# Kernel optimization log

Measured on AMD Instinct MI355X. Metric: run time of the kernel, lower is better.

The kernel has to match this reference:

```python
import jax, jax.numpy as jnp
import numpy as np

HIDDEN = 3072
HEADS = 24
HEAD_DIM = HIDDEN // HEADS  # 128
MLP_HIDDEN = 4 * HIDDEN     # 12288
IMG_LEN = 1024
TXT_LEN = 256
L = IMG_LEN + TXT_LEN
B = 1
EPS = 1e-6


def setup_inputs() -> dict:
    key = jax.random.key(0)
    ks = jax.random.split(key, 12)
    x = jax.random.normal(ks[0], (B, L, HIDDEN), jnp.float32)
    vec = jax.random.normal(ks[1], (B, HIDDEN), jnp.float32)
    # RoPE tables: real cos/sin of position * inv_freq, repeated over pairs (full head_dim)
    inv_freq = 1.0 / (10000.0 ** (np.arange(0, HEAD_DIM, 2, dtype=np.float32) / HEAD_DIM))
    theta = np.arange(IMG_LEN, dtype=np.float32)[:, None] * inv_freq[None, :]  # [img_len, D/2]
    theta = np.repeat(theta, 2, axis=-1)  # [img_len, D]
    freqs_cos = jnp.asarray(np.cos(theta))[None, :, None, :]  # [1, img_len, 1, D]
    freqs_sin = jnp.asarray(np.sin(theta))[None, :, None, :]
    s = 0.02
    mod_w = jax.random.normal(ks[2], (HIDDEN, 3 * HIDDEN), jnp.float32) * s
    mod_b = jnp.zeros((3 * HIDDEN,), jnp.float32)
    w1 = jax.random.normal(ks[3], (HIDDEN, 3 * HIDDEN + MLP_HIDDEN), jnp.float32) * s
    b1 = jnp.zeros((3 * HIDDEN + MLP_HIDDEN,), jnp.float32)
    w2 = jax.random.normal(ks[4], (HIDDEN + MLP_HIDDEN, HIDDEN), jnp.float32) * s
    b2 = jnp.zeros((HIDDEN,), jnp.float32)
    qn_w = jnp.ones((HEAD_DIM,), jnp.float32)
    kn_w = jnp.ones((HEAD_DIM,), jnp.float32)
    cu_seqlens_q = jnp.array([0, IMG_LEN, L], jnp.int32)
    cu_seqlens_kv = jnp.array([0, IMG_LEN, L], jnp.int32)
    return {"x": x, "vec": vec, "freqs_cos": freqs_cos, "freqs_sin": freqs_sin,
            "mod_w": mod_w, "mod_b": mod_b, "w1": w1, "b1": b1, "w2": w2, "b2": b2,
            "qn_w": qn_w, "kn_w": kn_w, "img_len": IMG_LEN,
            "cu_seqlens_q": cu_seqlens_q, "cu_seqlens_kv": cu_seqlens_kv}


def _layernorm(x):  # elementwise_affine=False
    mu = jnp.mean(x, axis=-1, keepdims=True)
    var = jnp.mean(jnp.square(x - mu), axis=-1, keepdims=True)
    return (x - mu) * jax.lax.rsqrt(var + EPS)


def _rmsnorm(x, w):
    ms = jnp.mean(jnp.square(x), axis=-1, keepdims=True)
    return x * jax.lax.rsqrt(ms + EPS) * w


def _rope_interleaved(x, cos, sin):
    # mode=1: rotate interleaved pairs: (-x1, x0, -x3, x2, ...)
    x0 = x[..., 0::2]
    x1 = x[..., 1::2]
    rot = jnp.stack([-x1, x0], axis=-1).reshape(x.shape)
    return x * cos + rot * sin


def reference(x, vec, freqs_cos, freqs_sin, mod_w, mod_b, w1, b1, w2, b2,
              qn_w, kn_w, img_len, cu_seqlens_q, cu_seqlens_kv):
    bs = x.shape[0]
    assert cu_seqlens_q.shape[0] == 2 * bs + 1
    # adaLN modulation: SiLU -> Linear(hidden, 3*hidden)
    mod = jax.nn.silu(vec) @ mod_w + mod_b           # [B, 3H]
    mod = mod[:, None, :]                             # [B, 1, 3H]
    mod_shift, mod_scale, mod_gate = jnp.split(mod, 3, axis=-1)
    x_mod = _layernorm(x) * (1.0 + mod_scale) + mod_shift
    # fused QKV + MLP projection
    h = x_mod @ w1 + b1                               # [B, L, 3*hidden + mlp]
    qkv = h[..., :3 * HIDDEN]
    mlp = h[..., 3 * HIDDEN:]
    # 'B L (K H D) -> K B L H D'
    qkv = qkv.reshape(bs, -1, 3, HEADS, HEAD_DIM)
    q, k, v = qkv[:, :, 0], qkv[:, :, 1], qkv[:, :, 2]  # [B, L, H, D]
    q = _rmsnorm(q, qn_w)
    k = _rmsnorm(k, kn_w)
    # RoPE on image tokens only
    img_q = _rope_interleaved(q[:, :img_len], freqs_cos, freqs_sin)
    img_k = _rope_interleaved(k[:, :img_len], freqs_cos, freqs_sin)
    q = jnp.concatenate([img_q, q[:, img_len:]], axis=1)
    k = jnp.concatenate([img_k, k[:, img_len:]], axis=1)
    # dense attention (bs==1 path, no mask), scale = 1/sqrt(head_dim)
    scale = 1.0 / jnp.sqrt(jnp.float32(HEAD_DIM))
    scores = jnp.einsum('bqhd,bkhd->bhqk', q, k) * scale
    probs = jax.nn.softmax(scores, axis=-1)
    attn = jnp.einsum('bhqk,bkhd->bqhd', probs, v)
    attn = attn.reshape(bs, -1, HEADS * HEAD_DIM)     # [B, L, hidden]
    # output projection on concat(attn, gelu_tanh(mlp))
    out = jnp.concatenate([attn, jax.nn.gelu(mlp, approximate=True)], axis=-1) @ w2 + b2
    return x + out * mod_gate
```

## Files before the change

### kernel.cpp

```cpp
#include <hip/hip_runtime.h>
#include <cstdint>
#include <cstddef>

typedef __bf16 bf16x8_t __attribute__((ext_vector_type(8)));
typedef float f32x4 __attribute__((ext_vector_type(4)));

#define HID 3072
#define NHEADS 24
#define HD 128
#define MLP 12288
#define SEQ 1280
#define IMG 1024
#define N1 21504
#define QKVW 9216
#define A2W 15360
#define EPSV 1e-6f

__device__ __forceinline__ size_t tpos(int row, int col, int KT) {
    return ((size_t)(row >> 8) * KT + (col >> 6)) * 16384
         + (size_t)(((((col >> 5) & 1) << 4) + ((row >> 4) & 15)) * 512
                    + (((row & 15) + (((col >> 3) & 3) << 4)) << 3) + (col & 7));
}

__device__ __forceinline__ void gload16(const void* g, void* l) {
    __builtin_amdgcn_global_load_lds(
        (const __attribute__((address_space(1))) unsigned int*)g,
        (__attribute__((address_space(3))) unsigned int*)l, 16, 0, 0);
}

__device__ __forceinline__ void bar() {
    asm volatile("" ::: "memory");
    __builtin_amdgcn_s_barrier();
    asm volatile("" ::: "memory");
}

__device__ __forceinline__ float bf2f(uint u) {
    return __builtin_bit_cast(float, u << 16);
}
__device__ __forceinline__ ushort f2bfu(float f) {
    return __builtin_bit_cast(ushort, (__bf16)f);
}

__device__ __forceinline__ void conv_tile(const float* __restrict__ in, ushort* __restrict__ out,
                                          int N, int KT, int kb, int nb, int tid,
                                          float (*tle)[65]) {
    int k0 = kb * 64, n0 = nb * 64;
    int rr = tid >> 2, cg = (tid & 3) * 16;
    #pragma unroll
    for (int j = 0; j < 4; ++j) {
        float4 vv = *reinterpret_cast<const float4*>(&in[(size_t)(k0 + rr) * N + n0 + cg + j * 4]);
        tle[rr][cg + j * 4 + 0] = vv.x;
        tle[rr][cg + j * 4 + 1] = vv.y;
        tle[rr][cg + j * 4 + 2] = vv.z;
        tle[rr][cg + j * 4 + 3] = vv.w;
    }
    __syncthreads();
    int nl = tid & 63;
    #pragma unroll
    for (int gg = 0; gg < 2; ++gg) {
        int g = (tid >> 6) + gg * 4;
        union { ushort u[8]; uint4 q; } pk;
        #pragma unroll
        for (int j = 0; j < 8; ++j)
            pk.u[j] = f2bfu(tle[g * 8 + j][nl]);
        *reinterpret_cast<uint4*>(&out[tpos(n0 + nl, k0 + g * 8, KT)]) = pk.q;
    }
}

__global__ void silu_kernel(const float* __restrict__ v, float* __restrict__ sv) {
    int i = blockIdx.x * 256 + threadIdx.x;
    float x = v[i];
    sv[i] = x / (1.f + expf(-x));
}

__global__ __launch_bounds__(256) void gemvconv_fat(const float* __restrict__ sv,
                                                    const float* __restrict__ W,
                                                    float* __restrict__ part,
                                                    const float* __restrict__ w1,
                                                    ushort* __restrict__ w1b) {
    __shared__ float tle[64][65];
    int bid = blockIdx.x;
    int tid = threadIdx.x;
    if (bid < 288) {
        int n = (bid % 36) * 256 + tid;
        int k0 = (bid / 36) * 384;
        float s = 0.f;
        for (int k = k0; k < k0 + 384; ++k)
            s = fmaf(sv[k], W[(size_t)k * QKVW + n], s);
        part[(size_t)(bid / 36) * QKVW + n] = s;
        return;
    }
    int cb = bid - 288;
    conv_tile(w1, w1b, N1, HID / 64, cb % 48, cb / 48, tid, tle);
}

__global__ void gemv_reduce(const float* __restrict__ part, const float* __restrict__ bias,
                            float* __restrict__ mod) {
    int n = blockIdx.x * 256 + threadIdx.x;
    float s = bias[n];
    #pragma unroll
    for (int ky = 0; ky < 8; ++ky) s += part[(size_t)ky * QKVW + n];
    mod[n] = s;
}

__global__ __launch_bounds__(384) void ln_mod_kernel(const float* __restrict__ x,
                                                     const float* __restrict__ mod,
                                                     ushort* __restrict__ xmt) {
    int m = blockIdx.x;
    int t = threadIdx.x;
    int lane = t & 63, w = t >> 6;
    const float* xr = x + (size_t)m * HID;
    float4 v0 = *reinterpret_cast<const float4*>(&xr[t * 8]);
    float4 v1 = *reinterpret_cast<const float4*>(&xr[t * 8 + 4]);
    float s = v0.x + v0.y + v0.z + v0.w + v1.x + v1.y + v1.z + v1.w;
    float sq = v0.x * v0.x + v0.y * v0.y + v0.z * v0.z + v0.w * v0.w +
               v1.x * v1.x + v1.y * v1.y + v1.z * v1.z + v1.w * v1.w;
    #pragma unroll
    for (int off = 1; off < 64; off <<= 1) {
        s += __shfl_xor(s, off);
        sq += __shfl_xor(sq, off);
    }
    __shared__ float red[12];
    if (lane == 0) { red[w] = s; red[w + 6] = sq; }
    __syncthreads();
    s = red[0] + red[1] + red[2] + red[3] + red[4] + red[5];
    sq = red[6] + red[7] + red[8] + red[9] + red[10] + red[11];
    float mu = s * (1.f / HID);
    float var = sq * (1.f / HID) - mu * mu;
    float rs = rsqrtf(var + EPSV);
    float vals[8] = {v0.x, v0.y, v0.z, v0.w, v1.x, v1.y, v1.z, v1.w};
    union { ushort u[8]; uint4 q; } pk;
    #pragma unroll
    for (int j = 0; j < 8; ++j) {
        int n = t * 8 + j;
        float y = (vals[j] - mu) * rs * (1.f + mod[HID + n]) + mod[n];
        pk.u[j] = f2bfu(y);
    }
    *reinterpret_cast<uint4*>(&xmt[tpos(m, t * 8, HID >> 6)]) = pk.q;
}

template <int EPI, int SPLITS>
__global__ __launch_bounds__(256, 2) void gemm128(
    const ushort* __restrict__ At, const ushort* __restrict__ Bt,
    const float* __restrict__ bias, ushort* __restrict__ out1, ushort* __restrict__ out2,
    int KT64, int NTloc, int NTN, int MB) {
    int nwg = gridDim.x;
    int q = nwg >> 3, r = nwg & 7;
    int orig = blockIdx.x;
    int xcd = orig & 7;
    int wgid = (xcd < r ? xcd * (q + 1) : r * (q + 1) + (xcd - r) * q) + (orig >> 3);
    int mt = wgid % MB;
    int p = wgid / MB;
    int nt = p % NTN;
    int sp = p / NTN;
    int kOff = sp * NTloc;
    int m0 = mt * 128, n0 = nt * 128;
    int hA = (mt & 1) * 8, hB = (nt & 1) * 8;

    __shared__ ushort LA[2][8192];
    __shared__ ushort LB[2][8192];

    int tid = threadIdx.x;
    int lane = tid & 63, wid = tid >> 6;
    int wm = wid >> 1, wn = wid & 1;
    int lr = lane & 15, lg = lane >> 4;

    const ushort* gA = At + (size_t)(mt >> 1) * KT64 * 16384;
    const ushort* gB = Bt + (size_t)(nt >> 1) * KT64 * 16384;

    f32x4 acc[4][4] = {};
    bf16x8_t af0[2][2], af1[2][2], bf0[2][2], bf1[2][2];

    auto stage = [&](ushort (*L)[8192], int buf, const ushort* g, int kt, int h0) {
        #pragma unroll
        for (int j = 0; j < 4; ++j) {
            int lb = wid * 4 + j;
            int b = ((lb >> 3) << 4) + h0 + (lb & 7);
            gload16(g + (size_t)kt * 16384 + b * 512 + lane * 8, &L[buf][lb * 512]);
        }
    };
    auto rdA = [&](int buf, int h, bf16x8_t (&af)[2][2]) {
        #pragma unroll
        for (int mi = 0; mi < 2; ++mi)
            #pragma unroll
            for (int k = 0; k < 2; ++k)
                af[mi][k] = *reinterpret_cast<const bf16x8_t*>(
                    &LA[buf][(k * 8 + wm * 4 + h * 2 + mi) * 512 + lane * 8]);
    };
    auto rdB = [&](int buf, int v, bf16x8_t (&bf)[2][2]) {
        #pragma unroll
        for (int ni = 0; ni < 2; ++ni)
            #pragma unroll
            for (int k = 0; k < 2; ++k)
                bf[ni][k] = *reinterpret_cast<const bf16x8_t*>(
                    &LB[buf][(k * 8 + wn * 4 + v * 2 + ni) * 512 + lane * 8]);
    };
    auto mmq = [&](bf16x8_t (&af)[2][2], bf16x8_t (&bf)[2][2], int h, int v) {
        __builtin_amdgcn_s_setprio(1);
        #pragma unroll
        for (int mi = 0; mi < 2; ++mi)
            #pragma unroll
            for (int ni = 0; ni < 2; ++ni)
                #pragma unroll
                for (int k = 0; k < 2; ++k)
                    acc[h * 2 + mi][v * 2 + ni] = __builtin_amdgcn_mfma_f32_16x16x32_bf16(
                        af[mi][k], bf[ni][k], acc[h * 2 + mi][v * 2 + ni], 0, 0, 0);
        __builtin_amdgcn_s_setprio(0);
    };

    stage(LA, 0, gA, kOff, hA);
    stage(LB, 0, gB, kOff, hB);
    stage(LA, 1, gA, kOff + 1, hA);
    stage(LB, 1, gB, kOff + 1, hB);
    asm volatile("s_waitcnt vmcnt(8)" ::: "memory");
    bar();
    rdA(0, 0, af0);
    rdB(0, 0, bf0);

    for (int t = 0; t < NTloc; ++t) {
        int c = t & 1;
        rdB(c, 1, bf1);
        mmq(af0, bf0, 0, 0);
        bar();
        rdA(c, 1, af1);
        mmq(af0, bf1, 0, 1);
        bar();
        if (t + 2 < NTloc) stage(LA, c, gA, kOff + t + 2, hA);
        mmq(af1, bf0, 1, 0);
        if (t + 1 < NTloc) {
            if (t + 2 < NTloc) asm volatile("s_waitcnt vmcnt(4)" ::: "memory");
            else               asm volatile("s_waitcnt vmcnt(0)" ::: "memory");
        }
        bar();
        if (t + 1 < NTloc) {
            rdA(c ^ 1, 0, af0);
            rdB(c ^ 1, 0, bf0);
        }
        if (t + 2 < NTloc) stage(LB, c, gB, kOff + t + 2, hB);
        mmq(af1, bf1, 1, 1);
        bar();
    }

    #pragma unroll
    for (int fi = 0; fi < 4; ++fi) {
        #pragma unroll
        for (int nj = 0; nj < 4; ++nj) {
            int col = n0 + wn * 64 + nj * 16 + lr;
            #pragma unroll
            for (int rr2 = 0; rr2 < 4; ++rr2) {
                int row = m0 + wm * 64 + fi * 16 + lg * 4 + rr2;
                float val = acc[fi][nj][rr2];
                if (EPI == 1) {
                    val += bias[col];
                    if (n0 < QKVW) {
                        out1[(size_t)row * QKVW + col] = f2bfu(val);
                    } else {
                        float u = 0.7978845608028654f * (val + 0.044715f * val * val * val);
                        float g = val / (1.f + __expf(-2.f * u));
                        out2[tpos(row, HID + (col - QKVW), A2W >> 6)] = f2bfu(g);
                    }
                } else {
                    out1[(size_t)(sp * SEQ + row) * HID + col] = f2bfu(val);
                }
            }
        }
    }
}

__global__ __launch_bounds__(256) void ksplit_reduce(const ushort* __restrict__ partb,
                                                     const float* __restrict__ x,
                                                     const float* __restrict__ bias,
                                                     const float* __restrict__ gate,
                                                     float* __restrict__ out) {
    size_t i = (size_t)blockIdx.x * 256 + threadIdx.x;
    int col = (int)((i * 8) % HID);
    float a[8] = {};
    #pragma unroll
    for (int s = 0; s < 4; ++s) {
        uint4 pv = *reinterpret_cast<const uint4*>(&partb[(size_t)s * SEQ * HID + i * 8]);
        uint w[4] = {pv.x, pv.y, pv.z, pv.w};
        #pragma unroll
        for (int c = 0; c < 4; ++c) {
            a[c * 2]     += bf2f(w[c] & 0xffffu);
            a[c * 2 + 1] += __builtin_bit_cast(float, w[c] & 0xffff0000u);
        }
    }
    f32x4 o0, o1;
    #pragma unroll
    for (int j = 0; j < 4; ++j) {
        o0[j] = x[i * 8 + j] + (a[j] + bias[col + j]) * gate[col + j];
        o1[j] = x[i * 8 + 4 + j] + (a[4 + j] + bias[col + 4 + j]) * gate[col + 4 + j];
    }
    *reinterpret_cast<f32x4*>(&out[i * 8]) = o0;
    *reinterpret_cast<f32x4*>(&out[i * 8 + 4]) = o1;
}

__global__ __launch_bounds__(256) void qkv_post(const ushort* __restrict__ hb,
                                                const float* __restrict__ fc,
                                                const float* __restrict__ fs,
                                                const float* __restrict__ qn,
                                                const float* __restrict__ kn,
                                                __bf16* __restrict__ qb,
                                                __bf16* __restrict__ kb,
                                                __bf16* __restrict__ vb) {
    int m = blockIdx.x;
    int lane = threadIdx.x & 63, w = threadIdx.x >> 6;
    for (int rr = w; rr < 72; rr += 4) {
        int s = rr / 24, hd = rr % 24;
        const ushort* src = hb + (size_t)m * QKVW + s * HID + hd * HD;
        uint pair = *reinterpret_cast<const uint*>(&src[2 * lane]);
        float x0 = bf2f(pair & 0xffffu);
        float x1 = __builtin_bit_cast(float, pair & 0xffff0000u);
        if (s < 2) {
            float ss = x0 * x0 + x1 * x1;
            #pragma unroll
            for (int off = 1; off < 64; off <<= 1) ss += __shfl_xor(ss, off);
            float rs = rsqrtf(ss * (1.f / HD) + EPSV);
            const float* nw = (s == 0) ? qn : kn;
            x0 *= rs * nw[2 * lane];
            x1 *= rs * nw[2 * lane + 1];
            if (m < IMG) {
                float c0 = fc[m * HD + 2 * lane], c1 = fc[m * HD + 2 * lane + 1];
                float s0 = fs[m * HD + 2 * lane], s1 = fs[m * HD + 2 * lane + 1];
                float r0 = x0 * c0 - x1 * s0;
                float r1 = x1 * c1 + x0 * s1;
                x0 = r0; x1 = r1;
            }
        }
        __bf16* dst = ((s == 0) ? qb : (s == 1) ? kb : vb) + (size_t)hd * SEQ * HD + (size_t)m * HD + 2 * lane;
        uint u0 = f2bfu(x0), u1 = f2bfu(x1);
        *reinterpret_cast<uint*>(dst) = u0 | (u1 << 16);
    }
}

__global__ __launch_bounds__(256) void attn_fat(const __bf16* __restrict__ qb,
                                                const __bf16* __restrict__ kb,
                                                const __bf16* __restrict__ vb,
                                                ushort* __restrict__ a2,
                                                const float* __restrict__ w2,
                                                ushort* __restrict__ w2b) {
    __shared__ float tle[64][65];
    int bid = blockIdx.x;
    int tid = threadIdx.x;
    if (bid >= 480) {
        int cb = bid - 480;
        conv_tile(w2, w2b, HID, A2W / 64, cb % 240, cb / 240, tid, tle);
        return;
    }
    __shared__ alignas(16) __bf16 Kl[32][136];
    __shared__ alignas(16) __bf16 Vl[32][136];
    __shared__ float Pl[4][32][16];

    int head = bid / 20;
    int lane = tid & 63, w = tid >> 6;
    int lr = lane & 15, lg = lane >> 4;
    int q0 = (bid % 20) * 64 + w * 16;
    const __bf16* Q = qb + (size_t)head * SEQ * HD;
    const __bf16* Kp = kb + (size_t)head * SEQ * HD;
    const __bf16* Vp = vb + (size_t)head * SEQ * HD;

    bf16x8_t qf[4];
    #pragma unroll
    for (int kc = 0; kc < 4; ++kc)
        qf[kc] = *reinterpret_cast<const bf16x8_t*>(&Q[(size_t)(q0 + lr) * HD + kc * 32 + lg * 8]);

    float m_run = -1e30f, l_run = 0.f;
    f32x4 of[8] = {};
    const float sm_scale = 0.08838834764831845f;

    for (int kv0 = 0; kv0 < SEQ; kv0 += 32) {
        #pragma unroll
        for (int cc = 0; cc < 2; ++cc) {
            int c = tid + cc * 256;
            int row = c >> 4, off = (c & 15) * 8;
            *reinterpret_cast<bf16x8_t*>(&Kl[row][off]) =
                *reinterpret_cast<const bf16x8_t*>(&Kp[(size_t)(kv0 + row) * HD + off]);
            *reinterpret_cast<bf16x8_t*>(&Vl[row][off]) =
                *reinterpret_cast<const bf16x8_t*>(&Vp[(size_t)(kv0 + row) * HD + off]);
        }
        __syncthreads();

        f32x4 st[2] = {};
        #pragma unroll
        for (int h = 0; h < 2; ++h)
            #pragma unroll
            for (int kc = 0; kc < 4; ++kc) {
                bf16x8_t kf = *reinterpret_cast<const bf16x8_t*>(&Kl[h * 16 + lr][kc * 32 + lg * 8]);
                st[h] = __builtin_amdgcn_mfma_f32_16x16x32_bf16(kf, qf[kc], st[h], 0, 0, 0);
            }
        float sarr[8];
        #pragma unroll
        for (int h = 0; h < 2; ++h)
            #pragma unroll
            for (int r = 0; r < 4; ++r) sarr[h * 4 + r] = st[h][r] * sm_scale;

        float mloc = sarr[0];
        #pragma unroll
        for (int i = 1; i < 8; ++i) mloc = fmaxf(mloc, sarr[i]);
        mloc = fmaxf(mloc, __shfl_xor(mloc, 16));
        mloc = fmaxf(mloc, __shfl_xor(mloc, 32));
        float m_new = fmaxf(m_run, mloc);
        float alpha = expf(m_run - m_new);
        float pv[8], psum = 0.f;
        #pragma unroll
        for (int i = 0; i < 8; ++i) { pv[i] = expf(sarr[i] - m_new); psum += pv[i]; }
        psum += __shfl_xor(psum, 16);
        psum += __shfl_xor(psum, 32);
        l_run = l_run * alpha + psum;
        m_run = m_new;

        #pragma unroll
        for (int h = 0; h < 2; ++h)
            #pragma unroll
            for (int r = 0; r < 4; ++r) Pl[w][h * 16 + lg * 4 + r][lr] = pv[h * 4 + r];
        bf16x8_t pa;
        #pragma unroll
        for (int j = 0; j < 8; ++j) pa[j] = (__bf16)Pl[w][lg * 8 + j][lr];

        float alr[4];
        #pragma unroll
        for (int r = 0; r < 4; ++r) alr[r] = __shfl(alpha, lg * 4 + r);

        #pragma unroll
        for (int db = 0; db < 8; ++db) {
            #pragma unroll
            for (int r = 0; r < 4; ++r) of[db][r] *= alr[r];
            bf16x8_t vv;
            #pragma unroll
            for (int j = 0; j < 8; ++j) vv[j] = Vl[lg * 8 + j][db * 16 + lr];
            of[db] = __builtin_amdgcn_mfma_f32_16x16x32_bf16(pa, vv, of[db], 0, 0, 0);
        }
        __syncthreads();
    }

    float lr4[4];
    #pragma unroll
    for (int r = 0; r < 4; ++r) lr4[r] = __shfl(l_run, lg * 4 + r);
    #pragma unroll
    for (int db = 0; db < 8; ++db)
        #pragma unroll
        for (int r = 0; r < 4; ++r) {
            int row = q0 + lg * 4 + r;
            int col = head * HD + db * 16 + lr;
            a2[tpos(row, col, A2W >> 6)] = f2bfu(of[db][r] / lr4[r]);
        }
}

extern "C" void kernel_launch(void* const* d_in, const int* in_sizes, int n_in,
                              void* d_out, int out_size, void* d_ws, size_t ws_size,
                              hipStream_t stream) {
    const float* x = (const float*)d_in[0];
    const float* vec = (const float*)d_in[1];
    const float* fc = (const float*)d_in[2];
    const float* fs = (const float*)d_in[3];
    const float* mod_w = (const float*)d_in[4];
    const float* mod_b = (const float*)d_in[5];
    const float* w1 = (const float*)d_in[6];
    const float* b1 = (const float*)d_in[7];
    const float* w2 = (const float*)d_in[8];
    const float* b2 = (const float*)d_in[9];
    const float* qn = (const float*)d_in[10];
    const float* kn = (const float*)d_in[11];
    float* out = (float*)d_out;

    char* ws = (char*)d_ws;
    size_t off = 0;
    float* sv = (float*)(ws + off); off += 3072 * 4;
    float* mod = (float*)(ws + off); off += 9216 * 4;
    float* part = (float*)(ws + off); off += 8 * 9216 * 4;
    off = (off + 255) & ~(size_t)255;
    ushort* xmt = (ushort*)(ws + off); off += (size_t)SEQ * HID * 2;
    off = (off + 255) & ~(size_t)255;
    ushort* hqkvb = (ushort*)(ws + off); off += (size_t)SEQ * QKVW * 2;
    __bf16* qb = (__bf16*)(ws + off); off += (size_t)NHEADS * SEQ * HD * 2;
    __bf16* kb = (__bf16*)(ws + off); off += (size_t)NHEADS * SEQ * HD * 2;
    __bf16* vb = (__bf16*)(ws + off); off += (size_t)NHEADS * SEQ * HD * 2;
    off = (off + 255) & ~(size_t)255;
    ushort* a2t = (ushort*)(ws + off); off += (size_t)SEQ * A2W * 2;
    ushort* partb = hqkvb;

    off = (off + 255) & ~(size_t)255;
    ushort* w1b = (ushort*)(ws + off);
    ushort* w2b = w1b;

    silu_kernel<<<12, 256, 0, stream>>>(vec, sv);
    gemvconv_fat<<<288 + 48 * 336, 256, 0, stream>>>(sv, mod_w, part, w1, w1b);
    gemv_reduce<<<36, 256, 0, stream>>>(part, mod_b, mod);
    ln_mod_kernel<<<SEQ, 384, 0, stream>>>(x, mod, xmt);

    gemm128<1, 1><<<10 * (N1 / 128), 256, 0, stream>>>(xmt, w1b, b1, hqkvb, a2t,
                                                       HID / 64, HID / 64, N1 / 128, 10);
    qkv_post<<<SEQ, 256, 0, stream>>>(hqkvb, fc, fs, qn, kn, qb, kb, vb);
    attn_fat<<<480 + 240 * 48, 256, 0, stream>>>(qb, kb, vb, a2t, w2, w2b);
    gemm128<2, 4><<<4 * 10 * (HID / 128), 256, 0, stream>>>(a2t, w2b, nullptr, partb, nullptr,
                                                            A2W / 64, A2W / 64 / 4, HID / 128, 10);
    ksplit_reduce<<<SEQ * HID / 2048, 256, 0, stream>>>(partb, x, b2, mod + 2 * HID, out);
}
```

Baseline: 702.3 us.

## Switch GEMMs to 256x256 tiles with 8-wave workgroups

Replaces the 128x128-tile, 4-wave GEMM with a 256x256-tile, 8-wave (512-thread) variant for both the QKV/MLP projection and the split-K output projection. Each wave now computes a 128x64 subtile, which raises data reuse per LDS load and halves global loads per output element. LDS use doubles to 128KB, accumulator registers double, and the grid shrinks (420 and 240 workgroups), so occupancy drops and there is more tail imbalance across CUs.

```diff
diff --git a/kernel.cpp b/kernel.cpp
--- a/kernel.cpp
+++ b/kernel.cpp
@@ -140,52 +140,50 @@
 }
 
 template <int EPI, int SPLITS>
-__global__ __launch_bounds__(256, 2) void gemm128(
+__global__ __launch_bounds__(512, 2) void gemm8p(
     const ushort* __restrict__ At, const ushort* __restrict__ Bt,
     const float* __restrict__ bias, ushort* __restrict__ out1, ushort* __restrict__ out2,
-    int KT64, int NTloc, int NTN, int MB) {
+    int KTtot, int NTloc, int NTN) {
     int nwg = gridDim.x;
     int q = nwg >> 3, r = nwg & 7;
     int orig = blockIdx.x;
     int xcd = orig & 7;
     int wgid = (xcd < r ? xcd * (q + 1) : r * (q + 1) + (xcd - r) * q) + (orig >> 3);
-    int mt = wgid % MB;
-    int p = wgid / MB;
+    int mt = wgid % 5;
+    int p = wgid / 5;
     int nt = p % NTN;
     int sp = p / NTN;
     int kOff = sp * NTloc;
-    int m0 = mt * 128, n0 = nt * 128;
-    int hA = (mt & 1) * 8, hB = (nt & 1) * 8;
-
-    __shared__ ushort LA[2][8192];
-    __shared__ ushort LB[2][8192];
+    int m0 = mt * 256, n0 = nt * 256;
+
+    __shared__ ushort LA[2][16384];
+    __shared__ ushort LB[2][16384];
 
     int tid = threadIdx.x;
     int lane = tid & 63, wid = tid >> 6;
-    int wm = wid >> 1, wn = wid & 1;
+    int wm = wid >> 2, wn = wid & 3;
     int lr = lane & 15, lg = lane >> 4;
 
-    const ushort* gA = At + (size_t)(mt >> 1) * KT64 * 16384;
-    const ushort* gB = Bt + (size_t)(nt >> 1) * KT64 * 16384;
-
-    f32x4 acc[4][4] = {};
-    bf16x8_t af0[2][2], af1[2][2], bf0[2][2], bf1[2][2];
-
-    auto stage = [&](ushort (*L)[8192], int buf, const ushort* g, int kt, int h0) {
+    const ushort* gA = At + (size_t)mt * KTtot * 16384;
+    const ushort* gB = Bt + (size_t)nt * KTtot * 16384;
+
+    f32x4 acc[8][4] = {};
+    bf16x8_t af0[4][2], af1[4][2], bf0[2][2], bf1[2][2];
+
+    auto stage = [&](ushort (*L)[16384], int buf, const ushort* g, int ktG) {
         #pragma unroll
         for (int j = 0; j < 4; ++j) {
-            int lb = wid * 4 + j;
-            int b = ((lb >> 3) << 4) + h0 + (lb & 7);
-            gload16(g + (size_t)kt * 16384 + b * 512 + lane * 8, &L[buf][lb * 512]);
+            int b = wid * 4 + j;
+            gload16(g + (size_t)ktG * 16384 + b * 512 + lane * 8, &L[buf][b * 512]);
         }
     };
-    auto rdA = [&](int buf, int h, bf16x8_t (&af)[2][2]) {
-        #pragma unroll
-        for (int mi = 0; mi < 2; ++mi)
+    auto rdA = [&](int buf, int h, bf16x8_t (&af)[4][2]) {
+        #pragma unroll
+        for (int mi = 0; mi < 4; ++mi)
             #pragma unroll
             for (int k = 0; k < 2; ++k)
                 af[mi][k] = *reinterpret_cast<const bf16x8_t*>(
-                    &LA[buf][(k * 8 + wm * 4 + h * 2 + mi) * 512 + lane * 8]);
+                    &LA[buf][(k * 16 + wm * 8 + h * 4 + mi) * 512 + lane * 8]);
     };
     auto rdB = [&](int buf, int v, bf16x8_t (&bf)[2][2]) {
         #pragma unroll
@@ -193,25 +191,25 @@
             #pragma unroll
             for (int k = 0; k < 2; ++k)
                 bf[ni][k] = *reinterpret_cast<const bf16x8_t*>(
-                    &LB[buf][(k * 8 + wn * 4 + v * 2 + ni) * 512 + lane * 8]);
+                    &LB[buf][(k * 16 + wn * 4 + v * 2 + ni) * 512 + lane * 8]);
     };
-    auto mmq = [&](bf16x8_t (&af)[2][2], bf16x8_t (&bf)[2][2], int h, int v) {
+    auto mmq = [&](bf16x8_t (&af)[4][2], bf16x8_t (&bf)[2][2], int h, int v) {
         __builtin_amdgcn_s_setprio(1);
         #pragma unroll
-        for (int mi = 0; mi < 2; ++mi)
+        for (int mi = 0; mi < 4; ++mi)
             #pragma unroll
             for (int ni = 0; ni < 2; ++ni)
                 #pragma unroll
                 for (int k = 0; k < 2; ++k)
-                    acc[h * 2 + mi][v * 2 + ni] = __builtin_amdgcn_mfma_f32_16x16x32_bf16(
-                        af[mi][k], bf[ni][k], acc[h * 2 + mi][v * 2 + ni], 0, 0, 0);
+                    acc[h * 4 + mi][v * 2 + ni] = __builtin_amdgcn_mfma_f32_16x16x32_bf16(
+                        af[mi][k], bf[ni][k], acc[h * 4 + mi][v * 2 + ni], 0, 0, 0);
         __builtin_amdgcn_s_setprio(0);
     };
 
-    stage(LA, 0, gA, kOff, hA);
-    stage(LB, 0, gB, kOff, hB);
-    stage(LA, 1, gA, kOff + 1, hA);
-    stage(LB, 1, gB, kOff + 1, hB);
+    stage(LA, 0, gA, kOff);
+    stage(LB, 0, gB, kOff);
+    stage(LA, 1, gA, kOff + 1);
+    stage(LB, 1, gB, kOff + 1);
     asm volatile("s_waitcnt vmcnt(8)" ::: "memory");
     bar();
     rdA(0, 0, af0);
@@ -225,7 +223,7 @@
         rdA(c, 1, af1);
         mmq(af0, bf1, 0, 1);
         bar();
-        if (t + 2 < NTloc) stage(LA, c, gA, kOff + t + 2, hA);
+        if (t + 2 < NTloc) stage(LA, c, gA, kOff + t + 2);
         mmq(af1, bf0, 1, 0);
         if (t + 1 < NTloc) {
             if (t + 2 < NTloc) asm volatile("s_waitcnt vmcnt(4)" ::: "memory");
@@ -236,20 +234,20 @@
             rdA(c ^ 1, 0, af0);
             rdB(c ^ 1, 0, bf0);
         }
-        if (t + 2 < NTloc) stage(LB, c, gB, kOff + t + 2, hB);
+        if (t + 2 < NTloc) stage(LB, c, gB, kOff + t + 2);
         mmq(af1, bf1, 1, 1);
         bar();
     }
 
     #pragma unroll
-    for (int fi = 0; fi < 4; ++fi) {
+    for (int mi8 = 0; mi8 < 8; ++mi8) {
         #pragma unroll
         for (int nj = 0; nj < 4; ++nj) {
             int col = n0 + wn * 64 + nj * 16 + lr;
             #pragma unroll
             for (int rr2 = 0; rr2 < 4; ++rr2) {
-                int row = m0 + wm * 64 + fi * 16 + lg * 4 + rr2;
-                float val = acc[fi][nj][rr2];
+                int row = m0 + wm * 128 + mi8 * 16 + lg * 4 + rr2;
+                float val = acc[mi8][nj][rr2];
                 if (EPI == 1) {
                     val += bias[col];
                     if (n0 < QKVW) {
@@ -488,11 +486,11 @@
     gemv_reduce<<<36, 256, 0, stream>>>(part, mod_b, mod);
     ln_mod_kernel<<<SEQ, 384, 0, stream>>>(x, mod, xmt);
 
-    gemm128<1, 1><<<10 * (N1 / 128), 256, 0, stream>>>(xmt, w1b, b1, hqkvb, a2t,
-                                                       HID / 64, HID / 64, N1 / 128, 10);
+    gemm8p<1, 1><<<5 * (N1 / 256), 512, 0, stream>>>(xmt, w1b, b1, hqkvb, a2t,
+                                                     HID / 64, HID / 64, N1 / 256);
     qkv_post<<<SEQ, 256, 0, stream>>>(hqkvb, fc, fs, qn, kn, qb, kb, vb);
     attn_fat<<<480 + 240 * 48, 256, 0, stream>>>(qb, kb, vb, a2t, w2, w2b);
-    gemm128<2, 4><<<4 * 10 * (HID / 128), 256, 0, stream>>>(a2t, w2b, nullptr, partb, nullptr,
-                                                            A2W / 64, A2W / 64 / 4, HID / 128, 10);
+    gemm8p<2, 4><<<4 * 5 * (HID / 256), 512, 0, stream>>>(a2t, w2b, nullptr, partb, nullptr,
+                                                          A2W / 64, A2W / 64 / 4, HID / 256);
     ksplit_reduce<<<SEQ * HID / 2048, 256, 0, stream>>>(partb, x, b2, mod + 2 * HID, out);
 }
```

Result: faster. 618.0 us (-12.0%).
